# Kernel optimization log

Hardware: AMD Instinct MI355X
Metric: run time of the kernel (lower is better)

The kernel has to match this reference:

```python
import jax, jax.numpy as jnp
import numpy as np

B, S, D, H = 2, 2048, 1024, 16
HD = D // H          # head_dim = 64
HALF = HD // 2       # rotary pair count = 32


def rope_freqs(seq_len, half, base=10000.0):
    # Llama-style: theta_j = base^(-2j/head_dim), angle m*theta_j
    inv = 1.0 / (base ** (np.arange(0, half, dtype=np.float32) / half))
    ang = np.arange(seq_len, dtype=np.float32)[:, None] * inv[None, :]  # [S, half]
    return jnp.asarray(np.cos(ang)), jnp.asarray(np.sin(ang))


def setup_inputs() -> dict:
    key = jax.random.key(0)
    kx, kq, kk, kv, ko = jax.random.split(key, 5)
    cos, sin = rope_freqs(S, HALF)  # real/imag of m_theta_polar_tensor
    s = 0.02
    return {
        "x": jax.random.normal(kx, (B, S, D), dtype=jnp.float32),
        "freqs_cos": cos,
        "freqs_sin": sin,
        "Wq": jax.random.normal(kq, (D, D), dtype=jnp.float32) * s,
        "Wk": jax.random.normal(kk, (D, D), dtype=jnp.float32) * s,
        "Wv": jax.random.normal(kv, (D, D), dtype=jnp.float32) * s,
        "Wout": jax.random.normal(ko, (D, D), dtype=jnp.float32) * s,
    }


def _apply_rope(t, cos, sin):
    # t: [B, S, H, HD]; rotate consecutive pairs (complex multiply)
    b, s, h, hd = t.shape
    tr = t.reshape(b, s, h, hd // 2, 2)
    t0, t1 = tr[..., 0], tr[..., 1]
    c = cos[None, :, None, :]  # [1, S, 1, HALF]
    sn = sin[None, :, None, :]
    o0 = t0 * c - t1 * sn
    o1 = t0 * sn + t1 * c
    return jnp.stack([o0, o1], axis=-1).reshape(b, s, h, hd)


def reference(x, freqs_cos, freqs_sin, Wq, Wk, Wv, Wout):
    b, s, _ = x.shape
    q = (x @ Wq).reshape(b, s, H, HD)
    k = (x @ Wk).reshape(b, s, H, HD)
    v = (x @ Wv).reshape(b, s, H, HD)
    q = _apply_rope(q, freqs_cos, freqs_sin)
    k = _apply_rope(k, freqs_cos, freqs_sin)
    # [B, H, S, S]
    scores = jnp.einsum("bqhd,bkhd->bhqk", q, k) / jnp.sqrt(jnp.float32(HD))
    causal = jnp.triu(jnp.ones((s, s), dtype=bool), k=1)
    scores = jnp.where(causal[None, None], -jnp.inf, scores)
    weights = jax.nn.softmax(scores, axis=-1)
    vectors = jnp.einsum("bhqk,bkhd->bqhd", weights, v).reshape(b, s, D)
    return vectors @ Wout
```

## Files before the change

kernel.cpp:

```cpp
#include <hip/hip_runtime.h>
#include <stdint.h>

typedef unsigned short u16;
typedef __attribute__((ext_vector_type(8))) short short8;
typedef __attribute__((ext_vector_type(4))) short short4v;
typedef __attribute__((ext_vector_type(4))) float f32x4;
typedef __attribute__((ext_vector_type(4))) unsigned short ushort4v;
typedef __attribute__((ext_vector_type(2))) unsigned int uint2v;

#define NB 2
#define NS 2048
#define ND 1024
#define NH 16
#define HDIM 64
#define NHALF 32
#define QSCALE 0.18033688f
#define NEGBIG -3.0e38f

__device__ __forceinline__ float bf2f(u16 u) {
  union { unsigned u; float f; } v; v.u = ((unsigned)u) << 16; return v.f;
}
__device__ __forceinline__ u16 f2bf(float f) {
  union { float f; unsigned u; } v; v.f = f;
  unsigned r = v.u + 0x7fffu + ((v.u >> 16) & 1u);
  return (u16)(r >> 16);
}

__device__ __forceinline__ unsigned cvt_pk_bf16(float lo, float hi) {
  unsigned r;
  asm("v_cvt_pk_bf16_f32 %0, %1, %2" : "=v"(r) : "v"(lo), "v"(hi));
  return r;
}

__device__ __forceinline__ void gld_lds16(const u16* g, u16* l) {
  void* gv = (void*)g;
  __builtin_amdgcn_global_load_lds((__attribute__((address_space(1))) void*)gv,
                                   (__attribute__((address_space(3))) void*)l, 16, 0, 0);
}

__global__ void cvt_x(const float* __restrict__ x, u16* __restrict__ xb) {
  int i = blockIdx.x * 256 + threadIdx.x;
  float4 v = ((const float4*)x)[i];
  ushort4v o;
  o.x = f2bf(v.x); o.y = f2bf(v.y); o.z = f2bf(v.z); o.w = f2bf(v.w);
  ((ushort4v*)xb)[i] = o;
}

__global__ void transpose_w3(const float* __restrict__ W0, const float* __restrict__ W1,
                             const float* __restrict__ W2, u16* __restrict__ dst0) {
  __shared__ float tile[32][33];
  const int z = blockIdx.z;
  const float* W = (z == 0) ? W0 : (z == 1) ? W1 : W2;
  u16* dst = dst0 + (size_t)z * ND * ND;
  const int n0 = blockIdx.x * 32, k0 = blockIdx.y * 32;
  const int tx = threadIdx.x, ty = threadIdx.y;
#pragma unroll
  for (int i = 0; i < 4; ++i)
    tile[ty + i * 8][tx] = W[(size_t)(k0 + ty + i * 8) * ND + n0 + tx];
  __syncthreads();
#pragma unroll
  for (int i = 0; i < 4; ++i)
    dst[(size_t)(n0 + ty + i * 8) * ND + k0 + tx] = f2bf(tile[tx][ty + i * 8]);
}

__global__ void transpose_w(const float* __restrict__ W, u16* __restrict__ dst) {
  __shared__ float tile[32][33];
  const int n0 = blockIdx.x * 32, k0 = blockIdx.y * 32;
  const int tx = threadIdx.x, ty = threadIdx.y;
#pragma unroll
  for (int i = 0; i < 4; ++i)
    tile[ty + i * 8][tx] = W[(size_t)(k0 + ty + i * 8) * ND + n0 + tx];
  __syncthreads();
#pragma unroll
  for (int i = 0; i < 4; ++i)
    dst[(size_t)(n0 + ty + i * 8) * ND + k0 + tx] = f2bf(tile[tx][ty + i * 8]);
}

__global__ void transpose_v(const u16* __restrict__ Vb, u16* __restrict__ VT) {
  __shared__ u16 tile[64][72];
  const int bh = blockIdx.y, s0 = blockIdx.x << 6;
  const int tid = threadIdx.x;
  const u16* src = Vb + ((size_t)bh * NS + s0) * HDIM;
  u16* dst = VT + (size_t)bh * HDIM * NS + s0;
#pragma unroll
  for (int it = 0; it < 2; ++it) {
    int i = it * 256 + tid;
    int s = i >> 3, d0 = (i & 7) << 3;
    *(short8*)&tile[s][d0] = *(const short8*)(src + (size_t)s * HDIM + d0);
  }
  __syncthreads();
#pragma unroll
  for (int it = 0; it < 2; ++it) {
    int i = it * 256 + tid;
    int d = i >> 3, ss0 = (i & 7) << 3;
    short8 v;
#pragma unroll
    for (int e = 0; e < 8; ++e) v[e] = tile[ss0 + e][d];
    *(short8*)(dst + (size_t)d * NS + ss0) = v;
  }
}

template<int MI, int MODE>
__global__ __launch_bounds__(256) void gemm64(
    const u16* __restrict__ A, const u16* __restrict__ BT,
    u16* __restrict__ qo, u16* __restrict__ ko, u16* __restrict__ vo,
    float* __restrict__ fo) {
  __shared__ u16 smem[MI * 2048 + 8192];
  const int tid = threadIdx.x;
  const int w = tid >> 6, lane = tid & 63;
  const int lr = lane & 15, lg = lane >> 4;
  const int bm = blockIdx.y * (MI * 32), bn = blockIdx.x << 7;
  const int wr = (w >> 1) * (MI * 16), wc = (w & 1) << 6;
  f32x4 acc[MI][4] = {};

  const int arow = tid >> 3;
  const int aslot = (tid & 7) ^ (arow & 7);
  const u16* ags = A + (size_t)(bm + arow) * ND + (aslot << 3);
  const u16* bgs = BT + (size_t)(bn + arow) * ND + (aslot << 3);
  u16* const As = smem;
  u16* const Bs = smem + MI * 2048;

  int af_off[MI][2], bf_off[4][2];
#pragma unroll
  for (int mi = 0; mi < MI; ++mi)
#pragma unroll
    for (int kk = 0; kk < 2; ++kk)
      af_off[mi][kk] = (wr + mi * 16 + lr) * 64 + ((((kk << 2) + lg) ^ (lr & 7)) << 3);
#pragma unroll
  for (int ni = 0; ni < 4; ++ni)
#pragma unroll
    for (int kk = 0; kk < 2; ++kk)
      bf_off[ni][kk] = (wc + ni * 16 + lr) * 64 + ((((kk << 2) + lg) ^ (lr & 7)) << 3);

  for (int kt = 0; kt < ND; kt += 64) {
#pragma unroll
    for (int it = 0; it < MI; ++it)
      gld_lds16(ags + it * (32 * ND) + kt, As + it * 2048 + w * 512);
#pragma unroll
    for (int it = 0; it < 4; ++it)
      gld_lds16(bgs + it * (32 * ND) + kt, Bs + it * 2048 + w * 512);
    __syncthreads();
#pragma unroll
    for (int kk = 0; kk < 2; ++kk) {
      short8 af[MI], bfr[4];
#pragma unroll
      for (int mi = 0; mi < MI; ++mi)
        af[mi] = *(const short8*)(As + af_off[mi][kk]);
#pragma unroll
      for (int ni = 0; ni < 4; ++ni)
        bfr[ni] = *(const short8*)(Bs + bf_off[ni][kk]);
#pragma unroll
      for (int mi = 0; mi < MI; ++mi)
#pragma unroll
        for (int ni = 0; ni < 4; ++ni)
          acc[mi][ni] = __builtin_amdgcn_mfma_f32_16x16x32_bf16(af[mi], bfr[ni], acc[mi][ni], 0, 0, 0);
    }
    __syncthreads();
  }

  if (MODE == 0) {
#pragma unroll
    for (int mi = 0; mi < MI; ++mi) {
#pragma unroll
      for (int ni = 0; ni < 4; ++ni) {
        const int n = bn + wc + ni * 16 + lr;
        const int which = n >> 10, hh = (n >> 6) & 15, d = n & 63;
        u16* dst = which == 0 ? qo : which == 1 ? ko : vo;
#pragma unroll
        for (int j = 0; j < 4; ++j) {
          const int m = bm + wr + mi * 16 + (lg << 2) + j;
          const int b = m >> 11, s = m & 2047;
          dst[(((size_t)(b * NH + hh) * NS + s) << 6) + d] = f2bf(acc[mi][ni][j]);
        }
      }
    }
  } else {
#pragma unroll
    for (int mi = 0; mi < MI; ++mi)
#pragma unroll
      for (int ni = 0; ni < 4; ++ni)
#pragma unroll
        for (int j = 0; j < 4; ++j) {
          const int m = bm + wr + mi * 16 + (lg << 2) + j;
          const int n = bn + wc + ni * 16 + lr;
          fo[(size_t)m * ND + n] = acc[mi][ni][j];
        }
  }
}

__global__ void rope_k(u16* __restrict__ Qb, u16* __restrict__ Kb,
                       const float* __restrict__ cosT, const float* __restrict__ sinT) {
  int t = blockIdx.x * 256 + threadIdx.x;
  int g = t & 7;
  int s = (t >> 3) & 2047;
  int bh = t >> 14;
  float4 c4 = *(const float4*)(cosT + s * NHALF + (g << 2));
  float4 s4 = *(const float4*)(sinT + s * NHALF + (g << 2));
  size_t off = (((size_t)bh * NS + s) << 6) + (g << 3);
  short8 q = *(const short8*)(Qb + off);
  short8 k = *(const short8*)(Kb + off);
  float cc[4] = {c4.x, c4.y, c4.z, c4.w}, ss[4] = {s4.x, s4.y, s4.z, s4.w};
  short8 qo, ko;
#pragma unroll
  for (int p = 0; p < 4; ++p) {
    float q0 = bf2f((u16)q[2 * p]), q1 = bf2f((u16)q[2 * p + 1]);
    qo[2 * p]     = (short)f2bf((q0 * cc[p] - q1 * ss[p]) * QSCALE);
    qo[2 * p + 1] = (short)f2bf((q0 * ss[p] + q1 * cc[p]) * QSCALE);
    float k0 = bf2f((u16)k[2 * p]), k1 = bf2f((u16)k[2 * p + 1]);
    ko[2 * p]     = (short)f2bf(k0 * cc[p] - k1 * ss[p]);
    ko[2 * p + 1] = (short)f2bf(k0 * ss[p] + k1 * cc[p]);
  }
  *(short8*)(Qb + off) = qo;
  *(short8*)(Kb + off) = ko;
}

__global__ __launch_bounds__(256, 4) void attn_k(
    const u16* __restrict__ Qb, const u16* __restrict__ Kb,
    const u16* __restrict__ VT, u16* __restrict__ Ob) {
  __shared__ u16 K2[2][4096];
  __shared__ u16 V2[2][4096];
  __shared__ u16 Pl[4][1024];
  const int tid = threadIdx.x, w = tid >> 6, lane = tid & 63;
  const int lr = lane & 15, lg = lane >> 4;
  const int bid = blockIdx.x;
  const int xcd = bid & 7, i = bid >> 3;
  const int bh = xcd * 4 + (i & 3);
  const int pair = i >> 2;
  const int b = bh >> 4, h = bh & 15;
  const u16* Qp = Qb + (size_t)bh * NS * HDIM;
  const u16* Kp = Kb + (size_t)bh * NS * HDIM;
  const u16* Vp = VT + (size_t)bh * NS * HDIM;

  int kf_off[4][2], vb_off[4][2], pw_off[4], pa_off[2];
#pragma unroll
  for (int u = 0; u < 4; ++u) {
    const int kvr = (u << 4) + lr;
#pragma unroll
    for (int c = 0; c < 2; ++c)
      kf_off[u][c] = kvr * 64 + ((((c << 6) + (lg << 4)) ^ ((kvr & 7) << 4)) >> 1);
  }
#pragma unroll
  for (int dn = 0; dn < 4; ++dn) {
    const int d = (dn << 4) + lr;
#pragma unroll
    for (int ks = 0; ks < 2; ++ks)
      vb_off[dn][ks] = d * 64 + ((((ks << 6) + (lg << 4)) ^ ((d & 7) << 4)) >> 1);
  }
#pragma unroll
  for (int u = 0; u < 4; ++u)
    pw_off[u] = lr * 64 + ((((u << 5) + (lg << 3)) ^ ((lr & 7) << 4)) >> 1);
#pragma unroll
  for (int ks = 0; ks < 2; ++ks)
    pa_off[ks] = lr * 64 + ((((ks << 6) + (lg << 4)) ^ ((lr & 7) << 4)) >> 1);
  u16* Pw = &Pl[w][0];

  const int rr = tid >> 3, slot = tid & 7;
  const int soff = (((slot << 4) ^ ((rr & 7) << 4)) >> 1);
  const u16* kg0 = Kp + rr * HDIM + soff;
  const u16* kg1 = Kp + (rr + 32) * HDIM + soff;
  const u16* vg0 = Vp + (size_t)rr * NS + soff;
  const u16* vg1 = Vp + (size_t)(rr + 32) * NS + soff;

#define STAGE(BUFI, KV0)                                         \
  {                                                              \
    gld_lds16(kg0 + (KV0) * HDIM, &K2[BUFI][w * 512]);           \
    gld_lds16(kg1 + (KV0) * HDIM, &K2[BUFI][(4 + w) * 512]);     \
    gld_lds16(vg0 + (KV0),        &V2[BUFI][w * 512]);           \
    gld_lds16(vg1 + (KV0),        &V2[BUFI][(4 + w) * 512]);     \
  }

#define STEP(BUF, KVT)                                                            \
  {                                                                               \
    const int kv0 = (KVT) << 6;                                                   \
    if ((KVT) + 1 < nst) STAGE(BUF ^ 1, kv0 + 64);                                \
    const u16* Kl = K2[BUF];                                                      \
    const u16* Vl = V2[BUF];                                                      \
    f32x4 st[4] = {};                                                             \
    __builtin_amdgcn_s_setprio(1);                                                \
    _Pragma("unroll") for (int u = 0; u < 4; ++u)                                 \
      _Pragma("unroll") for (int c = 0; c < 2; ++c)                               \
        st[u] = __builtin_amdgcn_mfma_f32_16x16x32_bf16(                          \
            *(const short8*)(Kl + kf_off[u][c]), qf[c], st[u], 0, 0, 0);          \
    __builtin_amdgcn_s_setprio(0);                                                \
    if (kv0 + 63 > qw) {                                                          \
      _Pragma("unroll") for (int u = 0; u < 4; ++u)                               \
        _Pragma("unroll") for (int j = 0; j < 4; ++j) {                           \
          const int kvg = kv0 + (u << 4) + (lg << 2) + j;                         \
          if (kvg > q_col) st[u][j] = NEGBIG;                                     \
        }                                                                         \
    }                                                                             \
    _Pragma("unroll") for (int u = 0; u < 4; ++u) {                               \
      const float e0 = __builtin_amdgcn_exp2f(st[u][0]);                          \
      const float e1 = __builtin_amdgcn_exp2f(st[u][1]);                          \
      const float e2 = __builtin_amdgcn_exp2f(st[u][2]);                          \
      const float e3 = __builtin_amdgcn_exp2f(st[u][3]);                          \
      lacc += (e0 + e1) + (e2 + e3);                                              \
      uint2v pk;                                                                  \
      pk.x = cvt_pk_bf16(e0, e1);                                                 \
      pk.y = cvt_pk_bf16(e2, e3);                                                 \
      *(uint2v*)(Pw + pw_off[u]) = pk;                                            \
    }                                                                             \
    {                                                                             \
      short8 pa0 = *(const short8*)(Pw + pa_off[0]);                              \
      short8 pa1 = *(const short8*)(Pw + pa_off[1]);                              \
      __builtin_amdgcn_s_setprio(1);                                              \
      _Pragma("unroll") for (int dn = 0; dn < 4; ++dn) {                          \
        o[dn] = __builtin_amdgcn_mfma_f32_16x16x32_bf16(                          \
            pa0, *(const short8*)(Vl + vb_off[dn][0]), o[dn], 0, 0, 0);           \
        o[dn] = __builtin_amdgcn_mfma_f32_16x16x32_bf16(                          \
            pa1, *(const short8*)(Vl + vb_off[dn][1]), o[dn], 0, 0, 0);           \
      }                                                                           \
      __builtin_amdgcn_s_setprio(0);                                              \
    }                                                                             \
    __syncthreads();                                                              \
  }

  for (int seg = 0; seg < 2; ++seg) {
    const int tile = seg ? pair : 31 - pair;
    const int q0 = tile << 6;
    const int qw = q0 + w * 16;
    const int q_col = qw + lr;
    const int nst = tile + 1;

    short8 qf[2];
#pragma unroll
    for (int c = 0; c < 2; ++c)
      qf[c] = *(const short8*)(Qp + (size_t)(qw + lr) * HDIM + c * 32 + lg * 8);

    f32x4 o[4] = {};
    float lacc = 0.f;

    STAGE(0, 0);
    __syncthreads();

    int kvt = 0;
    for (; kvt + 2 <= nst; kvt += 2) {
      STEP(0, kvt);
      STEP(1, kvt + 1);
    }
    if (kvt < nst) STEP(0, kvt);

    float rs = lacc;
    rs += __shfl_xor(rs, 16);
    rs += __shfl_xor(rs, 32);
    float li[4];
#pragma unroll
    for (int j = 0; j < 4; ++j) li[j] = 1.0f / __shfl(rs, (lg << 2) + j);
#pragma unroll
    for (int dn = 0; dn < 4; ++dn)
#pragma unroll
      for (int j = 0; j < 4; ++j) {
        const int m = b * NS + qw + (lg << 2) + j;
        const int col = h * 64 + dn * 16 + lr;
        Ob[(size_t)m * ND + col] = f2bf(o[dn][j] * li[j]);
      }
  }
}

extern "C" void kernel_launch(void* const* d_in, const int* in_sizes, int n_in,
                              void* d_out, int out_size, void* d_ws, size_t ws_size,
                              hipStream_t stream) {
  const float* x  = (const float*)d_in[0];
  const float* fc = (const float*)d_in[1];
  const float* fs = (const float*)d_in[2];
  const float* Wq = (const float*)d_in[3];
  const float* Wk = (const float*)d_in[4];
  const float* Wv = (const float*)d_in[5];
  const float* Wo = (const float*)d_in[6];
  float* out = (float*)d_out;
  char* ws = (char*)d_ws;

  u16* xb    = (u16*)(ws);
  u16* WTqkv = (u16*)(ws + (size_t)(8u << 20));
  u16* VT    = (u16*)(ws + (size_t)(8u << 20));
  u16* Qb    = (u16*)(ws + (size_t)(16u << 20));
  u16* Kb    = (u16*)(ws + (size_t)(24u << 20));
  u16* Vb    = (u16*)(ws + (size_t)(32u << 20));
  u16* WTo   = (u16*)(ws + (size_t)(32u << 20));
  u16* Ob    = xb;

  cvt_x<<<4096, 256, 0, stream>>>(x, xb);
  transpose_w3<<<dim3(32, 32, 3), dim3(32, 8), 0, stream>>>(Wq, Wk, Wv, WTqkv);
  gemm64<4, 0><<<dim3(24, 32), 256, 0, stream>>>(xb, WTqkv, Qb, Kb, Vb, nullptr);
  rope_k<<<2048, 256, 0, stream>>>(Qb, Kb, fc, fs);
  transpose_v<<<dim3(32, 32), 256, 0, stream>>>(Vb, VT);
  transpose_w<<<dim3(32, 32), dim3(32, 8), 0, stream>>>(Wo, WTo);
  attn_k<<<512, 256, 0, stream>>>(Qb, Kb, VT, Ob);
  gemm64<2, 1><<<dim3(8, 64), 256, 0, stream>>>(Ob, WTo, nullptr, nullptr, nullptr, out);
}
```

Before: 107.7 us.

## Give each attention wave two query tiles and merge weight transposes

The attention kernel now runs 128-thread blocks of two waves, and each wave handles 32 query rows as two 16-row fragments. Each K and V LDS fragment read therefore feeds two MFMAs, which cuts LDS traffic per FLOP. The K/V staging loop, the P scratch layout, masking and normalisation are reworked to match. Separately, the Wout transpose is folded into the QKV transpose launch and workspace buffers are reassigned, which removes one kernel launch. In exchange, the kernel keeps half as many waves resident per CU, so there is less latency hiding and more register pressure.

```diff
diff --git a/kernel.cpp b/kernel.cpp
--- a/kernel.cpp
+++ b/kernel.cpp
@@ -46,25 +46,13 @@
   ((ushort4v*)xb)[i] = o;
 }
 
-__global__ void transpose_w3(const float* __restrict__ W0, const float* __restrict__ W1,
-                             const float* __restrict__ W2, u16* __restrict__ dst0) {
+__global__ void transpose_w4(const float* __restrict__ W0, const float* __restrict__ W1,
+                             const float* __restrict__ W2, const float* __restrict__ W3,
+                             u16* __restrict__ dqkv, u16* __restrict__ dout) {
   __shared__ float tile[32][33];
   const int z = blockIdx.z;
-  const float* W = (z == 0) ? W0 : (z == 1) ? W1 : W2;
-  u16* dst = dst0 + (size_t)z * ND * ND;
-  const int n0 = blockIdx.x * 32, k0 = blockIdx.y * 32;
-  const int tx = threadIdx.x, ty = threadIdx.y;
-#pragma unroll
-  for (int i = 0; i < 4; ++i)
-    tile[ty + i * 8][tx] = W[(size_t)(k0 + ty + i * 8) * ND + n0 + tx];
-  __syncthreads();
-#pragma unroll
-  for (int i = 0; i < 4; ++i)
-    dst[(size_t)(n0 + ty + i * 8) * ND + k0 + tx] = f2bf(tile[tx][ty + i * 8]);
-}
-
-__global__ void transpose_w(const float* __restrict__ W, u16* __restrict__ dst) {
-  __shared__ float tile[32][33];
+  const float* W = (z == 0) ? W0 : (z == 1) ? W1 : (z == 2) ? W2 : W3;
+  u16* dst = (z < 3) ? (dqkv + (size_t)z * ND * ND) : dout;
   const int n0 = blockIdx.x * 32, k0 = blockIdx.y * 32;
   const int tx = threadIdx.x, ty = threadIdx.y;
 #pragma unroll
@@ -214,12 +202,12 @@
   *(short8*)(Kb + off) = ko;
 }
 
-__global__ __launch_bounds__(256, 4) void attn_k(
+__global__ __launch_bounds__(128) void attn_k(
     const u16* __restrict__ Qb, const u16* __restrict__ Kb,
     const u16* __restrict__ VT, u16* __restrict__ Ob) {
   __shared__ u16 K2[2][4096];
   __shared__ u16 V2[2][4096];
-  __shared__ u16 Pl[4][1024];
+  __shared__ u16 Pl[2][2048];
   const int tid = threadIdx.x, w = tid >> 6, lane = tid & 63;
   const int lr = lane & 15, lg = lane >> 4;
   const int bid = blockIdx.x;
@@ -231,7 +219,7 @@
   const u16* Kp = Kb + (size_t)bh * NS * HDIM;
   const u16* Vp = VT + (size_t)bh * NS * HDIM;
 
-  int kf_off[4][2], vb_off[4][2], pw_off[4], pa_off[2];
+  int kf_off[4][2], vb_off[4][2], pw_off[2][4], pa_off[2][2];
 #pragma unroll
   for (int u = 0; u < 4; ++u) {
     const int kvr = (u << 4) + lr;
@@ -247,26 +235,29 @@
       vb_off[dn][ks] = d * 64 + ((((ks << 6) + (lg << 4)) ^ ((d & 7) << 4)) >> 1);
   }
 #pragma unroll
-  for (int u = 0; u < 4; ++u)
-    pw_off[u] = lr * 64 + ((((u << 5) + (lg << 3)) ^ ((lr & 7) << 4)) >> 1);
-#pragma unroll
-  for (int ks = 0; ks < 2; ++ks)
-    pa_off[ks] = lr * 64 + ((((ks << 6) + (lg << 4)) ^ ((lr & 7) << 4)) >> 1);
+  for (int f = 0; f < 2; ++f) {
+#pragma unroll
+    for (int u = 0; u < 4; ++u)
+      pw_off[f][u] = (f * 16 + lr) * 64 + ((((u << 5) + (lg << 3)) ^ ((lr & 7) << 4)) >> 1);
+#pragma unroll
+    for (int ks = 0; ks < 2; ++ks)
+      pa_off[f][ks] = (f * 16 + lr) * 64 + ((((ks << 6) + (lg << 4)) ^ ((lr & 7) << 4)) >> 1);
+  }
   u16* Pw = &Pl[w][0];
 
-  const int rr = tid >> 3, slot = tid & 7;
-  const int soff = (((slot << 4) ^ ((rr & 7) << 4)) >> 1);
-  const u16* kg0 = Kp + rr * HDIM + soff;
-  const u16* kg1 = Kp + (rr + 32) * HDIM + soff;
-  const u16* vg0 = Vp + (size_t)rr * NS + soff;
-  const u16* vg1 = Vp + (size_t)(rr + 32) * NS + soff;
-
-#define STAGE(BUFI, KV0)                                         \
-  {                                                              \
-    gld_lds16(kg0 + (KV0) * HDIM, &K2[BUFI][w * 512]);           \
-    gld_lds16(kg1 + (KV0) * HDIM, &K2[BUFI][(4 + w) * 512]);     \
-    gld_lds16(vg0 + (KV0),        &V2[BUFI][w * 512]);           \
-    gld_lds16(vg1 + (KV0),        &V2[BUFI][(4 + w) * 512]);     \
+  const int rr8 = lane >> 3, slot = lane & 7;
+  const int soff = ((slot ^ rr8) << 3);
+  const int krow = w * 8 + rr8;
+  const u16* kbase = Kp + (size_t)krow * HDIM + soff;
+  const u16* vbase = Vp + (size_t)krow * NS + soff;
+
+#define STAGE(BUFI, KV0)                                                           \
+  {                                                                                \
+    _Pragma("unroll")                                                              \
+    for (int c = 0; c < 4; ++c) {                                                  \
+      gld_lds16(kbase + (size_t)((KV0) + c * 16) * HDIM, &K2[BUFI][c * 1024 + w * 512]); \
+      gld_lds16(vbase + (size_t)(c * 16) * NS + (KV0),   &V2[BUFI][c * 1024 + w * 512]); \
+    }                                                                              \
   }
 
 #define STEP(BUF, KVT)                                                            \
@@ -275,40 +266,62 @@
     if ((KVT) + 1 < nst) STAGE(BUF ^ 1, kv0 + 64);                                \
     const u16* Kl = K2[BUF];                                                      \
     const u16* Vl = V2[BUF];                                                      \
-    f32x4 st[4] = {};                                                             \
+    f32x4 st0[4] = {}, st1[4] = {};                                               \
     __builtin_amdgcn_s_setprio(1);                                                \
     _Pragma("unroll") for (int u = 0; u < 4; ++u)                                 \
-      _Pragma("unroll") for (int c = 0; c < 2; ++c)                               \
-        st[u] = __builtin_amdgcn_mfma_f32_16x16x32_bf16(                          \
-            *(const short8*)(Kl + kf_off[u][c]), qf[c], st[u], 0, 0, 0);          \
+      _Pragma("unroll") for (int c = 0; c < 2; ++c) {                             \
+        const short8 kf = *(const short8*)(Kl + kf_off[u][c]);                    \
+        st0[u] = __builtin_amdgcn_mfma_f32_16x16x32_bf16(kf, qf[0][c], st0[u], 0, 0, 0); \
+        st1[u] = __builtin_amdgcn_mfma_f32_16x16x32_bf16(kf, qf[1][c], st1[u], 0, 0, 0); \
+      }                                                                           \
     __builtin_amdgcn_s_setprio(0);                                                \
     if (kv0 + 63 > qw) {                                                          \
       _Pragma("unroll") for (int u = 0; u < 4; ++u)                               \
         _Pragma("unroll") for (int j = 0; j < 4; ++j) {                           \
           const int kvg = kv0 + (u << 4) + (lg << 2) + j;                         \
-          if (kvg > q_col) st[u][j] = NEGBIG;                                     \
+          if (kvg > qw + lr) st0[u][j] = NEGBIG;                                  \
+        }                                                                         \
+    }                                                                             \
+    if (kv0 + 63 > qw + 16) {                                                     \
+      _Pragma("unroll") for (int u = 0; u < 4; ++u)                               \
+        _Pragma("unroll") for (int j = 0; j < 4; ++j) {                           \
+          const int kvg = kv0 + (u << 4) + (lg << 2) + j;                         \
+          if (kvg > qw + 16 + lr) st1[u][j] = NEGBIG;                             \
         }                                                                         \
     }                                                                             \
     _Pragma("unroll") for (int u = 0; u < 4; ++u) {                               \
-      const float e0 = __builtin_amdgcn_exp2f(st[u][0]);                          \
-      const float e1 = __builtin_amdgcn_exp2f(st[u][1]);                          \
-      const float e2 = __builtin_amdgcn_exp2f(st[u][2]);                          \
-      const float e3 = __builtin_amdgcn_exp2f(st[u][3]);                          \
-      lacc += (e0 + e1) + (e2 + e3);                                              \
-      uint2v pk;                                                                  \
-      pk.x = cvt_pk_bf16(e0, e1);                                                 \
-      pk.y = cvt_pk_bf16(e2, e3);                                                 \
-      *(uint2v*)(Pw + pw_off[u]) = pk;                                            \
+      const float a0 = __builtin_amdgcn_exp2f(st0[u][0]);                         \
+      const float a1 = __builtin_amdgcn_exp2f(st0[u][1]);                         \
+      const float a2 = __builtin_amdgcn_exp2f(st0[u][2]);                         \
+      const float a3 = __builtin_amdgcn_exp2f(st0[u][3]);                         \
+      lacc0 += (a0 + a1) + (a2 + a3);                                             \
+      uint2v pk0;                                                                 \
+      pk0.x = cvt_pk_bf16(a0, a1);                                                \
+      pk0.y = cvt_pk_bf16(a2, a3);                                                \
+      *(uint2v*)(Pw + pw_off[0][u]) = pk0;                                        \
+      const float b0 = __builtin_amdgcn_exp2f(st1[u][0]);                         \
+      const float b1 = __builtin_amdgcn_exp2f(st1[u][1]);                         \
+      const float b2 = __builtin_amdgcn_exp2f(st1[u][2]);                         \
+      const float b3 = __builtin_amdgcn_exp2f(st1[u][3]);                         \
+      lacc1 += (b0 + b1) + (b2 + b3);                                             \
+      uint2v pk1;                                                                 \
+      pk1.x = cvt_pk_bf16(b0, b1);                                                \
+      pk1.y = cvt_pk_bf16(b2, b3);                                                \
+      *(uint2v*)(Pw + pw_off[1][u]) = pk1;                                        \
     }                                                                             \
     {                                                                             \
-      short8 pa0 = *(const short8*)(Pw + pa_off[0]);                              \
-      short8 pa1 = *(const short8*)(Pw + pa_off[1]);                              \
+      short8 pa00 = *(const short8*)(Pw + pa_off[0][0]);                          \
+      short8 pa01 = *(const short8*)(Pw + pa_off[0][1]);                          \
+      short8 pa10 = *(const short8*)(Pw + pa_off[1][0]);                          \
+      short8 pa11 = *(const short8*)(Pw + pa_off[1][1]);                          \
       __builtin_amdgcn_s_setprio(1);                                              \
       _Pragma("unroll") for (int dn = 0; dn < 4; ++dn) {                          \
-        o[dn] = __builtin_amdgcn_mfma_f32_16x16x32_bf16(                          \
-            pa0, *(const short8*)(Vl + vb_off[dn][0]), o[dn], 0, 0, 0);           \
-        o[dn] = __builtin_amdgcn_mfma_f32_16x16x32_bf16(                          \
-            pa1, *(const short8*)(Vl + vb_off[dn][1]), o[dn], 0, 0, 0);           \
+        const short8 vb0 = *(const short8*)(Vl + vb_off[dn][0]);                  \
+        const short8 vb1 = *(const short8*)(Vl + vb_off[dn][1]);                  \
+        o0[dn] = __builtin_amdgcn_mfma_f32_16x16x32_bf16(pa00, vb0, o0[dn], 0, 0, 0); \
+        o0[dn] = __builtin_amdgcn_mfma_f32_16x16x32_bf16(pa01, vb1, o0[dn], 0, 0, 0); \
+        o1[dn] = __builtin_amdgcn_mfma_f32_16x16x32_bf16(pa10, vb0, o1[dn], 0, 0, 0); \
+        o1[dn] = __builtin_amdgcn_mfma_f32_16x16x32_bf16(pa11, vb1, o1[dn], 0, 0, 0); \
       }                                                                           \
       __builtin_amdgcn_s_setprio(0);                                              \
     }                                                                             \
@@ -318,17 +331,18 @@
   for (int seg = 0; seg < 2; ++seg) {
     const int tile = seg ? pair : 31 - pair;
     const int q0 = tile << 6;
-    const int qw = q0 + w * 16;
-    const int q_col = qw + lr;
+    const int qw = q0 + w * 32;
     const int nst = tile + 1;
 
-    short8 qf[2];
-#pragma unroll
-    for (int c = 0; c < 2; ++c)
-      qf[c] = *(const short8*)(Qp + (size_t)(qw + lr) * HDIM + c * 32 + lg * 8);
-
-    f32x4 o[4] = {};
-    float lacc = 0.f;
+    short8 qf[2][2];
+#pragma unroll
+    for (int f = 0; f < 2; ++f)
+#pragma unroll
+      for (int c = 0; c < 2; ++c)
+        qf[f][c] = *(const short8*)(Qp + (size_t)(qw + f * 16 + lr) * HDIM + c * 32 + lg * 8);
+
+    f32x4 o0[4] = {}, o1[4] = {};
+    float lacc0 = 0.f, lacc1 = 0.f;
 
     STAGE(0, 0);
     __syncthreads();
@@ -340,19 +354,26 @@
     }
     if (kvt < nst) STEP(0, kvt);
 
-    float rs = lacc;
-    rs += __shfl_xor(rs, 16);
-    rs += __shfl_xor(rs, 32);
-    float li[4];
-#pragma unroll
-    for (int j = 0; j < 4; ++j) li[j] = 1.0f / __shfl(rs, (lg << 2) + j);
+    float rs0 = lacc0, rs1 = lacc1;
+    rs0 += __shfl_xor(rs0, 16);
+    rs0 += __shfl_xor(rs0, 32);
+    rs1 += __shfl_xor(rs1, 16);
+    rs1 += __shfl_xor(rs1, 32);
+    float li0[4], li1[4];
+#pragma unroll
+    for (int j = 0; j < 4; ++j) {
+      li0[j] = 1.0f / __shfl(rs0, (lg << 2) + j);
+      li1[j] = 1.0f / __shfl(rs1, (lg << 2) + j);
+    }
 #pragma unroll
     for (int dn = 0; dn < 4; ++dn)
 #pragma unroll
       for (int j = 0; j < 4; ++j) {
-        const int m = b * NS + qw + (lg << 2) + j;
         const int col = h * 64 + dn * 16 + lr;
-        Ob[(size_t)m * ND + col] = f2bf(o[dn][j] * li[j]);
+        const int m0 = b * NS + qw + (lg << 2) + j;
+        Ob[(size_t)m0 * ND + col] = f2bf(o0[dn][j] * li0[j]);
+        const int m1 = b * NS + qw + 16 + (lg << 2) + j;
+        Ob[(size_t)m1 * ND + col] = f2bf(o1[dn][j] * li1[j]);
       }
   }
 }
@@ -371,20 +392,19 @@
   char* ws = (char*)d_ws;
 
   u16* xb    = (u16*)(ws);
+  u16* VT    = (u16*)(ws);
   u16* WTqkv = (u16*)(ws + (size_t)(8u << 20));
-  u16* VT    = (u16*)(ws + (size_t)(8u << 20));
+  u16* WTo   = (u16*)(ws + (size_t)(14u << 20));
   u16* Qb    = (u16*)(ws + (size_t)(16u << 20));
   u16* Kb    = (u16*)(ws + (size_t)(24u << 20));
   u16* Vb    = (u16*)(ws + (size_t)(32u << 20));
-  u16* WTo   = (u16*)(ws + (size_t)(32u << 20));
-  u16* Ob    = xb;
+  u16* Ob    = Vb;
 
   cvt_x<<<4096, 256, 0, stream>>>(x, xb);
-  transpose_w3<<<dim3(32, 32, 3), dim3(32, 8), 0, stream>>>(Wq, Wk, Wv, WTqkv);
+  transpose_w4<<<dim3(32, 32, 4), dim3(32, 8), 0, stream>>>(Wq, Wk, Wv, Wo, WTqkv, WTo);
   gemm64<4, 0><<<dim3(24, 32), 256, 0, stream>>>(xb, WTqkv, Qb, Kb, Vb, nullptr);
   rope_k<<<2048, 256, 0, stream>>>(Qb, Kb, fc, fs);
   transpose_v<<<dim3(32, 32), 256, 0, stream>>>(Vb, VT);
-  transpose_w<<<dim3(32, 32), dim3(32, 8), 0, stream>>>(Wo, WTo);
-  attn_k<<<512, 256, 0, stream>>>(Qb, Kb, VT, Ob);
+  attn_k<<<512, 128, 0, stream>>>(Qb, Kb, VT, Ob);
   gemm64<2, 1><<<dim3(8, 64), 256, 0, stream>>>(Ob, WTo, nullptr, nullptr, nullptr, out);
 }
```

Measured after the change: 123.7 us. 1.15x slower.
